# Optimization experiments

Measured on AMD Instinct MI355X. Metric: run time of the kernel, lower is better.

Reference implementation:

```python
import jax, jax.numpy as jnp
import numpy as np

EPS = 1e-5

def bn(x, g, b):
    # BatchNorm1d, training-mode batch statistics.
    axes = (0, 2) if x.ndim == 3 else (0,)
    m = jnp.mean(x, axis=axes, keepdims=True)
    v = jnp.var(x, axis=axes, keepdims=True)
    shape = (1, -1, 1) if x.ndim == 3 else (1, -1)
    return (x - m) / jnp.sqrt(v + EPS) * g.reshape(shape) + b.reshape(shape)

def conv1(x, w):
    # 1x1 conv1d == channel matmul: w [O,C], x [B,C,N]
    return jnp.einsum('oc,bcn->bon', w, x)

def knn_cov(x, local_idx, k):
    # x: [B,C,N], local_idx: [B,N] bool (local=True branch)
    B, C, N = x.shape
    xx = jnp.sum(x * x, axis=1, keepdims=True)          # [B,1,N]
    inner = -2.0 * jnp.einsum('bcn,bcm->bnm', x, x)      # [B,N,N]
    pd = -xx - inner - jnp.swapaxes(xx, 1, 2)            # neg sq dist [B,N,N]
    Min = jnp.min(pd, axis=-1)                           # [B,N]
    pd = jnp.where(local_idx[:, None, :], pd, Min[:, :, None])
    idx = jax.lax.top_k(jax.lax.stop_gradient(pd), k)[1]  # [B,N,k] nearest
    pts = jnp.swapaxes(x, 1, 2)                          # [B,N,C]
    knn_x = jax.vmap(lambda p, i: p[i])(pts, idx)        # [B,N,k,C]
    knn_x = knn_x - jnp.mean(knn_x, axis=2, keepdims=True)
    cov = jnp.einsum('bnkc,bnkd->bncd', knn_x, knn_x)    # [B,N,C,C]
    cov = cov.reshape(B, N, C * C).transpose(0, 2, 1)    # [B,C^2,N]
    return jnp.concatenate([x, cov], axis=1)             # [B,C+C^2,N]

def setup_inputs() -> dict:
    key = jax.random.key(0)
    ks = jax.random.split(key, 16)
    B, C, N, k = 4, 3, 8192, 20
    emb = 1024
    d = {}
    d['x'] = jax.random.normal(ks[0], (B, C, N), dtype=jnp.float32)
    d['local_idx'] = jax.random.randint(ks[1], (B, N), 0, 2) > 0
    d['k'] = k
    cin = C + C * C  # 12
    d['w1'] = jax.random.normal(ks[2], (64, cin), jnp.float32) * 0.1
    d['w2'] = jax.random.normal(ks[3], (64, 64), jnp.float32) * 0.1
    d['w3'] = jax.random.normal(ks[4], (64, 64), jnp.float32) * 0.1
    d['w4'] = jax.random.normal(ks[5], (128, 64), jnp.float32) * 0.1
    d['w5'] = jax.random.normal(ks[6], (emb, 128), jnp.float32) * 0.05
    for i, c in zip(range(1, 6), [64, 64, 64, 128, emb]):
        d[f'g{i}'] = jnp.ones((c,), jnp.float32)
        d[f'b{i}'] = jnp.zeros((c,), jnp.float32)
    d['lw1'] = jax.random.normal(ks[7], (512, emb), jnp.float32) * 0.03
    d['g6'] = jnp.ones((512,), jnp.float32)
    d['b6'] = jnp.zeros((512,), jnp.float32)
    d['lw2'] = jax.random.normal(ks[8], (4, 512), jnp.float32) * 0.05
    d['lb2'] = jnp.zeros((4,), jnp.float32)
    return d

def reference(x, local_idx, k, w1, w2, w3, w4, w5,
              g1, b1, g2, b2, g3, b3, g4, b4, g5, b5,
              lw1, g6, b6, lw2, lb2):
    h = knn_cov(x, local_idx, k)                 # [B,12,N]
    h = jax.nn.relu(bn(conv1(h, w1), g1, b1))
    h = jax.nn.relu(bn(conv1(h, w2), g2, b2))
    h = jax.nn.relu(bn(conv1(h, w3), g3, b3))
    h = jax.nn.relu(bn(conv1(h, w4), g4, b4))
    h = jax.nn.relu(bn(conv1(h, w5), g5, b5))    # [B,emb,N]
    h = jnp.max(h, axis=2)                        # global max pool [B,emb]
    h = jax.nn.relu(bn(h @ lw1.T, g6, b6))        # [B,512]
    # dropout: identity at eval
    return h @ lw2.T + lb2                        # [B,4]
```

## Files before the change

### kernel.cpp

```cpp
#include <hip/hip_runtime.h>

constexpr int BB = 4, NN = 8192, KNB = 20;
constexpr int BN_ = BB * NN;
constexpr float EPSV = 1e-5f;

constexpr size_t OFF_MODE  = 0;
constexpr size_t OFF_PCNT  = 16;
constexpr size_t OFF_PL    = 64;
constexpr size_t OFF_M0 = OFF_PL + 131072;
constexpr size_t OFF_S0 = OFF_M0 + 12;
constexpr size_t OFF_M1 = OFF_S0 + 144;
constexpr size_t OFF_S1 = OFF_M1 + 64;
constexpr size_t OFF_M2 = OFF_S1 + 64 * 64;
constexpr size_t OFF_S2 = OFF_M2 + 64;
constexpr size_t OFF_M3 = OFF_S2 + 64 * 64;
constexpr size_t OFF_S3 = OFF_M3 + 64;
constexpr size_t OFF_M4 = OFF_S3 + 64 * 64;
constexpr size_t OFF_S4 = OFF_M4 + 128;
constexpr size_t OFF_POOL = OFF_S4 + 128 * 128;
constexpr size_t OFF_ZEND = OFF_POOL + BB * 1024;
constexpr size_t OFF_A1 = OFF_ZEND;
constexpr size_t OFF_B1 = OFF_A1 + 64;
constexpr size_t OFF_A2 = OFF_B1 + 64;
constexpr size_t OFF_B2 = OFF_A2 + 64;
constexpr size_t OFF_A3 = OFF_B2 + 64;
constexpr size_t OFF_B3 = OFF_A3 + 64;
constexpr size_t OFF_A4 = OFF_B3 + 64;
constexpr size_t OFF_B4 = OFF_A4 + 128;
constexpr size_t OFF_A5 = OFF_B4 + 128;
constexpr size_t OFF_B5 = OFF_A5 + 1024;
constexpr size_t OFF_SH = OFF_B5 + 1024;
constexpr size_t OFF_WT1 = OFF_SH + BB * 512;
constexpr size_t OFF_WT2 = OFF_WT1 + 768;
constexpr size_t OFF_WT3 = OFF_WT2 + 4096;
constexpr size_t OFF_WT4 = OFF_WT3 + 4096;
constexpr size_t OFF_WT5_RAW = OFF_WT4 + 8192;
constexpr size_t OFF_WT5 = (OFF_WT5_RAW + 63) & ~size_t(63);
constexpr size_t OFF_H0_RAW = OFF_WT5 + 1024 * 128;
constexpr size_t OFF_H0 = (OFF_H0_RAW + 63) & ~size_t(63);
constexpr size_t OFF_H1 = OFF_H0 + (size_t)BB * 12 * NN;
constexpr size_t OFF_H2 = OFF_H1 + (size_t)BB * 64 * NN;
constexpr size_t OFF_H3 = OFF_H1;
constexpr size_t OFF_H4 = OFF_H2 + (size_t)BB * 64 * NN;
constexpr size_t OFF_P64  = OFF_H4;
constexpr size_t OFF_P128 = OFF_H1;
constexpr size_t WS_FLOATS = OFF_H4 + (size_t)BB * 128 * NN;

__device__ inline float dist3(const float4 c, float x0, float x1, float x2) {
  const float d0 = c.x - x0, d1 = c.y - x1, d2 = c.z - x2;
  return __builtin_fmaf(d0, d0, __builtin_fmaf(d1, d1, d2 * d2));
}

__global__ __launch_bounds__(256) void k_prep(const unsigned int* __restrict__ li32,
                                              int* __restrict__ mode,
                                              int* __restrict__ pcnt,
                                              float4* __restrict__ pl,
                                              const float* __restrict__ x) {
  const int b = blockIdx.x;
  const int t = threadIdx.x;
  const int lane = t & 63;
  const int w = t >> 6;
  __shared__ int s_wc[4];
  __shared__ int s_base;
  __shared__ int s_any;
  if (t == 0) { s_base = 0; s_any = 0; }
  __syncthreads();
  unsigned int any = 0;
  for (int i = t; i < 2048; i += 256) any |= (li32[b * 2048 + i] > 1u) ? 1u : 0u;
  if (any) atomicOr(&s_any, 1);
  __syncthreads();
  const int md = s_any;
  if (b == 0 && t == 0) *mode = md;
  const unsigned char* p8 = (const unsigned char*)li32;
  const float* __restrict__ xb = x + (size_t)b * 3 * NN;
  for (int j0 = 0; j0 < NN; j0 += 256) {
    const int m = j0 + t;
    const int f = md ? (p8[b * NN + m] != 0) : (li32[b * NN + m] != 0);
    const unsigned long long mask = __ballot(f);
    const int pos = __popcll(mask & ((1ull << lane) - 1ull));
    if (lane == 0) s_wc[w] = (int)__popcll(mask);
    __syncthreads();
    int off = s_base;
    for (int ww = 0; ww < w; ++ww) off += s_wc[ww];
    const int tot = s_wc[0] + s_wc[1] + s_wc[2] + s_wc[3];
    if (f) pl[(size_t)b * NN + off + pos] =
        make_float4(xb[m], xb[NN + m], xb[2 * NN + m], __int_as_float(m));
    __syncthreads();
    if (t == 0) s_base += tot;
    __syncthreads();
  }
  if (t == 0) pcnt[b] = s_base;
}

__global__ void k_wtall(const float* __restrict__ w1, const float* __restrict__ w2,
                        const float* __restrict__ w3, const float* __restrict__ w4,
                        const float* __restrict__ w5, float* __restrict__ wt1,
                        float* __restrict__ wt2, float* __restrict__ wt3,
                        float* __restrict__ wt4, float* __restrict__ wt5) {
  const int i = blockIdx.x * 256 + threadIdx.x;
  if (i < 768)        { const int o = i / 12,  c = i % 12;  wt1[c * 64 + o]  = w1[i]; }
  else if (i < 4864)  { const int j = i - 768;  const int o = j >> 6, c = j & 63;  wt2[c * 64 + o]  = w2[j]; }
  else if (i < 8960)  { const int j = i - 4864; const int o = j >> 6, c = j & 63;  wt3[c * 64 + o]  = w3[j]; }
  else if (i < 17152) { const int j = i - 8960; const int o = j >> 6, c = j & 63;  wt4[c * 128 + o] = w4[j]; }
  else if (i < 148224){ const int j = i - 17152;const int o = j >> 7, c = j & 127; wt5[c * 1024 + o] = w5[j]; }
}

__global__ __launch_bounds__(512) void k_knn(const float* __restrict__ x,
                                             const float4* __restrict__ pl,
                                             const int* __restrict__ pcnt,
                                             float* __restrict__ h0) {
  const int blk  = blockIdx.x;
  const int b    = blk >> 7;
  const int tile = blk & 127;
  const int t    = threadIdx.x;
  const int lane = t & 63;
  const int w    = __builtin_amdgcn_readfirstlane(t >> 6);
  const int n    = tile * 64 + lane;

  __shared__ float s_pool[8 * 64 * 21];
  __shared__ float s_T[64];
  __shared__ float s_red[64][13];
  __shared__ int   s_tc[64];
  __shared__ int   s_ti[64][16];
  float* __restrict__ s_dbuf  = s_pool;
  int*   __restrict__ s_dbufi = (int*)s_pool;

  const float* __restrict__ xb  = x + (size_t)b * 3 * NN;
  const float4* __restrict__ plb = pl + (size_t)b * NN;
  const int cnt = pcnt[b];
  const float xn0 = xb[n], xn1 = xb[NN + n], xn2 = xb[2 * NN + n];

  const int jlo = (cnt * w) >> 3;
  const int jhi = (cnt * (w + 1)) >> 3;

  float tk[KNB];
#pragma unroll
  for (int i = 0; i < KNB; ++i) tk[i] = 3.0e38f;

  {
    float thr = 3.0e38f;
    int bc = 0;
    for (int j = jlo; j < jhi; ++j) {
      const float4 c = plb[j];
      const float d = dist3(c, xn0, xn1, xn2);
      if (d < thr) { s_dbuf[bc * 512 + t] = d; ++bc; }
      if (__any(bc == 8)) {
        for (int i = 0; i < bc; ++i) {
          float dv = s_dbuf[i * 512 + t];
          if (dv < tk[KNB - 1]) {
#pragma unroll
            for (int q2 = 0; q2 < KNB; ++q2) {
              const float lo = fminf(tk[q2], dv);
              dv = fmaxf(tk[q2], dv);
              tk[q2] = lo;
            }
          }
        }
        bc = 0;
        thr = tk[KNB - 1];
      }
    }
    for (int i = 0; i < bc; ++i) {
      float dv = s_dbuf[i * 512 + t];
      if (dv < tk[KNB - 1]) {
#pragma unroll
        for (int q2 = 0; q2 < KNB; ++q2) {
          const float lo = fminf(tk[q2], dv);
          dv = fmaxf(tk[q2], dv);
          tk[q2] = lo;
        }
      }
    }
  }
  __syncthreads();

  {
    const int base = (w * 64 + lane) * 21;
#pragma unroll
    for (int i = 0; i < KNB; ++i) s_pool[base + i] = tk[i];
    s_pool[base + KNB] = 3.0e38f;
  }
  __syncthreads();

  if (w == 0) {
    int i0 = 0, i1 = 0, i2 = 0, i3 = 0, i4 = 0, i5 = 0, i6 = 0, i7 = 0;
    float T = 0.f;
    for (int c = 0; c < KNB; ++c) {
      const float v0 = s_pool[(0 * 64 + lane) * 21 + i0];
      const float v1 = s_pool[(1 * 64 + lane) * 21 + i1];
      const float v2 = s_pool[(2 * 64 + lane) * 21 + i2];
      const float v3 = s_pool[(3 * 64 + lane) * 21 + i3];
      const float v4 = s_pool[(4 * 64 + lane) * 21 + i4];
      const float v5 = s_pool[(5 * 64 + lane) * 21 + i5];
      const float v6 = s_pool[(6 * 64 + lane) * 21 + i6];
      const float v7 = s_pool[(7 * 64 + lane) * 21 + i7];
      float best = fminf(fminf(fminf(v0, v1), fminf(v2, v3)),
                         fminf(fminf(v4, v5), fminf(v6, v7)));
      int adv, taken;
      adv = (v0 == best) ? 1 : 0;           i0 += adv; taken = adv;
      adv = (!taken && v1 == best) ? 1 : 0; i1 += adv; taken |= adv;
      adv = (!taken && v2 == best) ? 1 : 0; i2 += adv; taken |= adv;
      adv = (!taken && v3 == best) ? 1 : 0; i3 += adv; taken |= adv;
      adv = (!taken && v4 == best) ? 1 : 0; i4 += adv; taken |= adv;
      adv = (!taken && v5 == best) ? 1 : 0; i5 += adv; taken |= adv;
      adv = (!taken && v6 == best) ? 1 : 0; i6 += adv; taken |= adv;
      adv = (!taken && v7 == best) ? 1 : 0; i7 += adv;
      T = best;
    }
    s_T[lane] = T;
    s_tc[lane] = 0;
  }
  __syncthreads();
  const float T = s_T[lane];

  float sx = 0, sy = 0, sz = 0;
  float xx = 0, xy = 0, xz = 0, yy = 0, yz = 0, zz = 0;
  float clf = 0;
  {
    s_dbufi[t] = jlo;
    int bc = 0;
    for (int j = jlo; j < jhi; ++j) {
      const float4 c = plb[j];
      const float d = dist3(c, xn0, xn1, xn2);
      if (d <= T) { s_dbufi[bc * 512 + t] = j; ++bc; }
      if (__any(bc == 8)) {
        int jj[8]; float4 cc[8];
#pragma unroll
        for (int i = 0; i < 8; ++i) {
          const int slot = (i < bc) ? i : 0;
          jj[i] = s_dbufi[slot * 512 + t];
          cc[i] = plb[jj[i]];
        }
#pragma unroll
        for (int i = 0; i < 8; ++i) {
          if (i < bc) {
            const float d2 = dist3(cc[i], xn0, xn1, xn2);
            if (d2 < T) {
              clf += 1.f;
              sx += cc[i].x; sy += cc[i].y; sz += cc[i].z;
              xx = __builtin_fmaf(cc[i].x, cc[i].x, xx);
              xy = __builtin_fmaf(cc[i].x, cc[i].y, xy);
              xz = __builtin_fmaf(cc[i].x, cc[i].z, xz);
              yy = __builtin_fmaf(cc[i].y, cc[i].y, yy);
              yz = __builtin_fmaf(cc[i].y, cc[i].z, yz);
              zz = __builtin_fmaf(cc[i].z, cc[i].z, zz);
            } else {
              const int pos = atomicAdd(&s_tc[lane], 1);
              if (pos < 16) s_ti[lane][pos] = jj[i];
            }
          }
        }
        bc = 0;
      }
    }
    if (bc > 0) {
      int jj[8]; float4 cc[8];
#pragma unroll
      for (int i = 0; i < 8; ++i) {
        const int slot = (i < bc) ? i : 0;
        jj[i] = s_dbufi[slot * 512 + t];
        cc[i] = plb[jj[i]];
      }
#pragma unroll
      for (int i = 0; i < 8; ++i) {
        if (i < bc) {
          const float d2 = dist3(cc[i], xn0, xn1, xn2);
          if (d2 < T) {
            clf += 1.f;
            sx += cc[i].x; sy += cc[i].y; sz += cc[i].z;
            xx = __builtin_fmaf(cc[i].x, cc[i].x, xx);
            xy = __builtin_fmaf(cc[i].x, cc[i].y, xy);
            xz = __builtin_fmaf(cc[i].x, cc[i].z, xz);
            yy = __builtin_fmaf(cc[i].y, cc[i].y, yy);
            yz = __builtin_fmaf(cc[i].y, cc[i].z, yz);
            zz = __builtin_fmaf(cc[i].z, cc[i].z, zz);
          } else {
            const int pos = atomicAdd(&s_tc[lane], 1);
            if (pos < 16) s_ti[lane][pos] = jj[i];
          }
        }
      }
    }
  }
  __syncthreads();
  {
    const int base = (w * 64 + lane) * 13;
    s_pool[base + 0] = sx; s_pool[base + 1] = sy; s_pool[base + 2] = sz;
    s_pool[base + 3] = xx; s_pool[base + 4] = xy; s_pool[base + 5] = xz;
    s_pool[base + 6] = yy; s_pool[base + 7] = yz; s_pool[base + 8] = zz;
    s_pool[base + 9] = clf;
  }
  __syncthreads();
  {
    const int q = t & 63, a = t >> 6;
    float s = 0.f;
#pragma unroll
    for (int wv = 0; wv < 8; ++wv) s += s_pool[(wv * 64 + q) * 13 + a];
    s_red[q][a] = s;
    if (a < 2) {
      const int a2 = a + 8;
      float s2 = 0.f;
#pragma unroll
      for (int wv = 0; wv < 8; ++wv) s2 += s_pool[(wv * 64 + q) * 13 + a2];
      s_red[q][a2] = s2;
    }
  }
  __syncthreads();

  if (w == 0) {
    float fsx = s_red[lane][0], fsy = s_red[lane][1], fsz = s_red[lane][2];
    float fxx = s_red[lane][3], fxy = s_red[lane][4], fxz = s_red[lane][5];
    float fyy = s_red[lane][6], fyz = s_red[lane][7], fzz = s_red[lane][8];
    const int cl = (int)s_red[lane][9];
    const int r = KNB - cl;
    const int tc = min(s_tc[lane], 16);
    int kk = cl;
    int prev = -1;
    for (int s = 0; s < r; ++s) {
      int best = 0x7fffffff;
      for (int u = 0; u < tc; ++u) {
        const int mi2 = s_ti[lane][u];
        if (mi2 > prev && mi2 < best) best = mi2;
      }
      if (best == 0x7fffffff) break;
      const float4 pp = plb[best];
      fsx += pp.x; fsy += pp.y; fsz += pp.z;
      fxx = __builtin_fmaf(pp.x, pp.x, fxx);
      fxy = __builtin_fmaf(pp.x, pp.y, fxy);
      fxz = __builtin_fmaf(pp.x, pp.z, fxz);
      fyy = __builtin_fmaf(pp.y, pp.y, fyy);
      fyz = __builtin_fmaf(pp.y, pp.z, fyz);
      fzz = __builtin_fmaf(pp.z, pp.z, fzz);
      prev = best;
      ++kk;
    }
    const float kf = (float)max(kk, 1);
    const float inv = 1.0f / kf;
    const float mx = fsx * inv, my = fsy * inv, mz = fsz * inv;
    const float c00 = fxx - kf * mx * mx;
    const float c01 = fxy - kf * mx * my;
    const float c02 = fxz - kf * mx * mz;
    const float c11 = fyy - kf * my * my;
    const float c12 = fyz - kf * my * mz;
    const float c22 = fzz - kf * mz * mz;
    float* __restrict__ op = h0 + (size_t)b * 12 * NN + n;
    op[0] = xn0; op[(size_t)NN] = xn1; op[(size_t)2 * NN] = xn2;
    op[(size_t)3 * NN] = c00; op[(size_t)4 * NN]  = c01; op[(size_t)5 * NN]  = c02;
    op[(size_t)6 * NN] = c01; op[(size_t)7 * NN]  = c11; op[(size_t)8 * NN]  = c12;
    op[(size_t)9 * NN] = c02; op[(size_t)10 * NN] = c12; op[(size_t)11 * NN] = c22;
  }
}

template <int C>
__global__ __launch_bounds__(256) void k_stats_small(const float* __restrict__ h,
                                                     float* __restrict__ mo,
                                                     float* __restrict__ So) {
  constexpr int NP  = C * (C + 1) / 2;
  constexpr int KPT = (NP + 255) / 256;
  __shared__ float tile[C][65];
  const int t = threadIdx.x;
  float acc[KPT];
#pragma unroll
  for (int e = 0; e < KPT; ++e) acc[e] = 0.f;
  float accm = 0.f;
  for (int tl = blockIdx.x; tl < BN_ / 64; tl += gridDim.x) {
    const int b  = tl >> 7;
    const int p0 = (tl & 127) * 64;
    for (int idx = t; idx < C * 64; idx += 256) {
      const int c = idx >> 6, p = idx & 63;
      tile[c][p] = h[((size_t)b * C + c) * NN + p0 + p];
    }
    __syncthreads();
    {
      int ii = 0, rem = t;
#pragma unroll
      for (int e = 0; e < KPT; ++e) {
        const int lin = t + 256 * e;
        if (lin < NP) {
          while (rem >= C - ii) { rem -= C - ii; ++ii; }
          const int jj = ii + rem;
          float s = 0.f;
#pragma unroll 8
          for (int p = 0; p < 64; ++p) s = __builtin_fmaf(tile[ii][p], tile[jj][p], s);
          acc[e] += s;
        }
        rem += 256;
      }
    }
    if (t < C) {
      float s = 0.f;
#pragma unroll 8
      for (int p = 0; p < 64; ++p) s += tile[t][p];
      accm += s;
    }
    __syncthreads();
  }
  {
    int ii = 0, rem = t;
#pragma unroll
    for (int e = 0; e < KPT; ++e) {
      const int lin = t + 256 * e;
      if (lin < NP) {
        while (rem >= C - ii) { rem -= C - ii; ++ii; }
        atomicAdd(&So[ii * C + ii + rem], acc[e]);
      }
      rem += 256;
    }
  }
  if (t < C) atomicAdd(&mo[t], accm);
}

template <int C>
__global__ __launch_bounds__(512) void k_stats(const float* __restrict__ h,
                                               float* __restrict__ part) {
  constexpr int G      = (C == 128) ? 8 : 4;
  constexpr int NPB    = 136 * G * G;
  constexpr int ROWLEN = NPB + C;
  constexpr int STR    = C + 4;
  __shared__ float ht[128][STR];
  __shared__ float red[136][G * G];
  const int t   = threadIdx.x;
  const int blk = blockIdx.x;
  const int b   = blk >> 6;
  const int p0  = (blk & 63) * 128;
  for (int i = t; i < C * 128; i += 512) {
    const int c = i >> 7, p = i & 127;
    ht[p][c] = h[((size_t)b * C + c) * NN + p0 + p];
  }
  __syncthreads();
  const int s  = t >> 8;
  const int pb = t & 255;
  const int bi = pb & 15;
  const int bj = pb >> 4;
  const bool act = (bi <= bj);
  float acc[G * G];
#pragma unroll
  for (int g = 0; g < G * G; ++g) acc[g] = 0.f;
  if (act) {
    for (int p = s * 64; p < s * 64 + 64; ++p) {
      float a[G], bv[G];
      *(float4*)&a[0] = *(const float4*)&ht[p][bi * G];
      *(float4*)&bv[0] = *(const float4*)&ht[p][bj * G];
      if constexpr (G == 8) {
        *(float4*)&a[4] = *(const float4*)&ht[p][bi * G + 4];
        *(float4*)&bv[4] = *(const float4*)&ht[p][bj * G + 4];
      }
#pragma unroll
      for (int gi = 0; gi < G; ++gi)
#pragma unroll
        for (int gj = 0; gj < G; ++gj)
          acc[gi * G + gj] = __builtin_fmaf(a[gi], bv[gj], acc[gi * G + gj]);
    }
  }
  const int rank = bj * (bj + 1) / 2 + bi;
  if (s == 1 && act) {
#pragma unroll
    for (int g = 0; g < G * G; ++g) red[rank][g] = acc[g];
  }
  __syncthreads();
  float* __restrict__ prow = part + (size_t)blk * ROWLEN;
  if (s == 0 && act) {
#pragma unroll
    for (int g = 0; g < G * G; g += 4) {
      float4 v;
      v.x = acc[g + 0] + red[rank][g + 0];
      v.y = acc[g + 1] + red[rank][g + 1];
      v.z = acc[g + 2] + red[rank][g + 2];
      v.w = acc[g + 3] + red[rank][g + 3];
      *(float4*)&prow[rank * G * G + g] = v;
    }
  }
  if (t < C) {
    float sm = 0.f;
#pragma unroll 8
    for (int p = 0; p < 128; ++p) sm += ht[p][t];
    prow[NPB + t] = sm;
  }
}

template <int C>
__global__ __launch_bounds__(256) void k_sred(const float* __restrict__ part,
                                              float* __restrict__ mo,
                                              float* __restrict__ So) {
  constexpr int G      = (C == 128) ? 8 : 4;
  constexpr int GG     = G * G;
  constexpr int NPB    = 136 * GG;
  constexpr int ROWLEN = NPB + C;
  const int e = blockIdx.x * 256 + threadIdx.x;
  if (e >= ROWLEN) return;
  const float* __restrict__ p = part + e;
  float s = 0.f;
#pragma unroll 8
  for (int r = 0; r < 256; ++r) s += p[(size_t)r * ROWLEN];
  if (e < NPB) {
    const int rank = e / GG;
    const int g    = e - rank * GG;
    int bj = 0;
    while ((bj + 1) * (bj + 2) / 2 <= rank) ++bj;
    const int bi = rank - bj * (bj + 1) / 2;
    const int gi = g / G, gj = g - gi * G;
    So[(bi * G + gi) * C + (bj * G + gj)] = s;
  } else {
    mo[e - NPB] = s;
  }
}

template <int CIN, int COUT>
__global__ __launch_bounds__(256) void k_solve(const float* __restrict__ w, const float* __restrict__ g,
                        const float* __restrict__ bb, const float* __restrict__ m,
                        const float* __restrict__ S, float* __restrict__ A,
                        float* __restrict__ Bc) {
  const int wv   = threadIdx.x >> 6;
  const int lane = threadIdx.x & 63;
  const int o    = blockIdx.x * 4 + wv;
  if (o >= COUT) return;
  const float* __restrict__ wr = w + (size_t)o * CIN;
  float mu = 0.f;
  for (int i = lane; i < CIN; i += 64) mu = __builtin_fmaf(wr[i], m[i], mu);
  float e2 = 0.f;
#pragma unroll 4
  for (int lin = lane; lin < CIN * CIN; lin += 64) {
    const int i = lin / CIN;
    const int j = lin - i * CIN;
    const int lo = min(i, j), hi = max(i, j);
    e2 = __builtin_fmaf(wr[i] * wr[j], S[lo * CIN + hi], e2);
  }
#pragma unroll
  for (int off = 32; off >= 1; off >>= 1) {
    mu += __shfl_xor(mu, off, 64);
    e2 += __shfl_xor(e2, off, 64);
  }
  if (lane == 0) {
    mu *= (1.0f / BN_);
    e2 *= (1.0f / BN_);
    const float var = e2 - mu * mu;
    const float a = g[o] / sqrtf(var + EPSV);
    A[o] = a;
    Bc[o] = bb[o] - mu * a;
  }
}

template <int CIN, int COUT>
__global__ __launch_bounds__(256) void k_cgemm(const float* __restrict__ hin,
                                               const float* __restrict__ wt,
                                               const float* __restrict__ A,
                                               const float* __restrict__ Bc,
                                               float* __restrict__ outp) {
  constexpr int nOT = COUT / 64;
  __shared__ float tin[CIN][64];
  __shared__ float twt[CIN][64];
  const int blk = blockIdx.x;
  const int ot  = blk % nOT;
  const int pt  = blk / nOT;
  const int b   = pt >> 7;
  const int p0  = (pt & 127) * 64;
  const int o0  = ot * 64;
  const int t   = threadIdx.x;

  for (int i = t; i < CIN * 16; i += 256) {
    const int c = i >> 4, sgm = i & 15;
    *(float4*)&tin[c][sgm * 4] =
        *(const float4*)&hin[((size_t)b * CIN + c) * NN + p0 + sgm * 4];
    *(float4*)&twt[c][sgm * 4] =
        *(const float4*)&wt[(size_t)c * COUT + o0 + sgm * 4];
  }
  __syncthreads();

  const int to = t & 15;
  const int tp = t >> 4;
  float acc[4][4];
#pragma unroll
  for (int i = 0; i < 4; ++i)
#pragma unroll
    for (int j = 0; j < 4; ++j) acc[i][j] = 0.f;

#pragma unroll 4
  for (int c = 0; c < CIN; ++c) {
    const float4 av = *(const float4*)&twt[c][to * 4];
    const float4 pv = *(const float4*)&tin[c][tp * 4];
    const float aa[4] = {av.x, av.y, av.z, av.w};
    const float pp[4] = {pv.x, pv.y, pv.z, pv.w};
#pragma unroll
    for (int i = 0; i < 4; ++i)
#pragma unroll
      for (int j = 0; j < 4; ++j)
        acc[i][j] = __builtin_fmaf(aa[i], pp[j], acc[i][j]);
  }

#pragma unroll
  for (int i = 0; i < 4; ++i) {
    const int o = o0 + to * 4 + i;
    const float Ao = A[o], Bo = Bc[o];
    float4 vv;
    vv.x = fmaxf(__builtin_fmaf(acc[i][0], Ao, Bo), 0.f);
    vv.y = fmaxf(__builtin_fmaf(acc[i][1], Ao, Bo), 0.f);
    vv.z = fmaxf(__builtin_fmaf(acc[i][2], Ao, Bo), 0.f);
    vv.w = fmaxf(__builtin_fmaf(acc[i][3], Ao, Bo), 0.f);
    *(float4*)&outp[((size_t)b * COUT + o) * NN + p0 + tp * 4] = vv;
  }
}

__global__ __launch_bounds__(256) void k_cgemm5(const float* __restrict__ h4,
                                                const float* __restrict__ wt,
                                                const float* __restrict__ A,
                                                const float* __restrict__ Bc,
                                                float* __restrict__ pooled) {
  __shared__ float tin[64][64];
  __shared__ float twt[64][128];
  const int blk = blockIdx.x;
  const int ot  = blk & 7;
  const int pt  = blk >> 3;
  const int b   = pt >> 7;
  const int p0  = (pt & 127) * 64;
  const int o0  = ot * 128;
  const int t   = threadIdx.x;
  const int to  = t & 15;
  const int tp  = t >> 4;

  float acc[8][4];
#pragma unroll
  for (int i = 0; i < 8; ++i)
#pragma unroll
    for (int j = 0; j < 4; ++j) acc[i][j] = 0.f;

  for (int kc = 0; kc < 128; kc += 64) {
    if (kc) __syncthreads();
    for (int i = t; i < 64 * 16; i += 256) {
      const int c = i >> 4, sg = i & 15;
      *(float4*)&tin[c][sg * 4] =
          *(const float4*)&h4[((size_t)b * 128 + kc + c) * NN + p0 + sg * 4];
    }
    for (int i = t; i < 64 * 32; i += 256) {
      const int c = i >> 5, sg = i & 31;
      *(float4*)&twt[c][sg * 4] =
          *(const float4*)&wt[(size_t)(kc + c) * 1024 + o0 + sg * 4];
    }
    __syncthreads();
#pragma unroll 2
    for (int c = 0; c < 64; ++c) {
      float w8[8], p4[4];
      *(float4*)&w8[0] = *(const float4*)&twt[c][to * 8];
      *(float4*)&w8[4] = *(const float4*)&twt[c][to * 8 + 4];
      *(float4*)&p4[0] = *(const float4*)&tin[c][tp * 4];
#pragma unroll
      for (int i = 0; i < 8; ++i)
#pragma unroll
        for (int j = 0; j < 4; ++j)
          acc[i][j] = __builtin_fmaf(w8[i], p4[j], acc[i][j]);
    }
  }

  float mx[8];
#pragma unroll
  for (int i = 0; i < 8; ++i) {
    const int o = o0 + to * 8 + i;
    const float a = A[o], bo = Bc[o];
    float v0 = fmaxf(__builtin_fmaf(acc[i][0], a, bo), 0.f);
    float v1 = fmaxf(__builtin_fmaf(acc[i][1], a, bo), 0.f);
    float v2 = fmaxf(__builtin_fmaf(acc[i][2], a, bo), 0.f);
    float v3 = fmaxf(__builtin_fmaf(acc[i][3], a, bo), 0.f);
    float m = fmaxf(fmaxf(v0, v1), fmaxf(v2, v3));
    m = fmaxf(m, __shfl_xor(m, 16, 64));
    m = fmaxf(m, __shfl_xor(m, 32, 64));
    mx[i] = m;
  }
  float* s_part = &twt[0][0];
  __syncthreads();
  const int lane = t & 63, w = t >> 6;
  if (lane < 16) {
#pragma unroll
    for (int i = 0; i < 8; ++i) s_part[w * 128 + to * 8 + i] = mx[i];
  }
  __syncthreads();
  if (t < 128) {
    const float mm = fmaxf(fmaxf(s_part[t], s_part[128 + t]),
                           fmaxf(s_part[256 + t], s_part[384 + t]));
    atomicMax((int*)pooled + (size_t)b * 1024 + o0 + t, __float_as_int(mm));
  }
}

__global__ __launch_bounds__(256) void k_head1(const float* __restrict__ pooled, const float* __restrict__ lw1,
                        const float* __restrict__ g6, const float* __restrict__ b6,
                        float* __restrict__ sh) {
  const int wv   = threadIdx.x >> 6;
  const int lane = threadIdx.x & 63;
  const int o    = blockIdx.x * 4 + wv;
  const float* __restrict__ wr = lw1 + (size_t)o * 1024;
  float y0 = 0, y1 = 0, y2 = 0, y3 = 0;
  for (int c = lane; c < 1024; c += 64) {
    const float wvv = wr[c];
    y0 = __builtin_fmaf(wvv, pooled[c], y0);
    y1 = __builtin_fmaf(wvv, pooled[1024 + c], y1);
    y2 = __builtin_fmaf(wvv, pooled[2048 + c], y2);
    y3 = __builtin_fmaf(wvv, pooled[3072 + c], y3);
  }
#pragma unroll
  for (int off = 32; off >= 1; off >>= 1) {
    y0 += __shfl_xor(y0, off, 64);
    y1 += __shfl_xor(y1, off, 64);
    y2 += __shfl_xor(y2, off, 64);
    y3 += __shfl_xor(y3, off, 64);
  }
  if (lane == 0) {
    const float mu = 0.25f * (y0 + y1 + y2 + y3);
    const float d0 = y0 - mu, d1 = y1 - mu, d2 = y2 - mu, d3 = y3 - mu;
    const float var = 0.25f * (d0 * d0 + d1 * d1 + d2 * d2 + d3 * d3);
    const float a = g6[o] / sqrtf(var + EPSV);
    const float bc = b6[o];
    sh[o]        = fmaxf(__builtin_fmaf(d0, a, bc), 0.f);
    sh[512 + o]  = fmaxf(__builtin_fmaf(d1, a, bc), 0.f);
    sh[1024 + o] = fmaxf(__builtin_fmaf(d2, a, bc), 0.f);
    sh[1536 + o] = fmaxf(__builtin_fmaf(d3, a, bc), 0.f);
  }
}

__global__ void k_head2(const float* __restrict__ sh, const float* __restrict__ lw2,
                        const float* __restrict__ lb2, float* __restrict__ out) {
  const int wv   = threadIdx.x >> 6;
  const int lane = threadIdx.x & 63;
  float s0 = 0, s1 = 0, s2 = 0, s3 = 0;
  for (int c = lane; c < 512; c += 64) {
    const float h = sh[wv * 512 + c];
    s0 = __builtin_fmaf(lw2[c], h, s0);
    s1 = __builtin_fmaf(lw2[512 + c], h, s1);
    s2 = __builtin_fmaf(lw2[1024 + c], h, s2);
    s3 = __builtin_fmaf(lw2[1536 + c], h, s3);
  }
#pragma unroll
  for (int off = 32; off >= 1; off >>= 1) {
    s0 += __shfl_xor(s0, off, 64);
    s1 += __shfl_xor(s1, off, 64);
    s2 += __shfl_xor(s2, off, 64);
    s3 += __shfl_xor(s3, off, 64);
  }
  if (lane == 0) {
    out[wv * 4 + 0] = s0 + lb2[0];
    out[wv * 4 + 1] = s1 + lb2[1];
    out[wv * 4 + 2] = s2 + lb2[2];
    out[wv * 4 + 3] = s3 + lb2[3];
  }
}

extern "C" void kernel_launch(void* const* d_in, const int* in_sizes, int n_in,
                              void* d_out, int out_size, void* d_ws, size_t ws_size,
                              hipStream_t stream) {
  (void)in_sizes; (void)n_in; (void)out_size; (void)ws_size;
  const float* x    = (const float*)d_in[0];
  const void*  lidx = d_in[1];
  const float* w1 = (const float*)d_in[3];
  const float* w2 = (const float*)d_in[4];
  const float* w3 = (const float*)d_in[5];
  const float* w4 = (const float*)d_in[6];
  const float* w5 = (const float*)d_in[7];
  const float* g1 = (const float*)d_in[8],  *b1 = (const float*)d_in[9];
  const float* g2 = (const float*)d_in[10], *b2 = (const float*)d_in[11];
  const float* g3 = (const float*)d_in[12], *b3 = (const float*)d_in[13];
  const float* g4 = (const float*)d_in[14], *b4 = (const float*)d_in[15];
  const float* g5 = (const float*)d_in[16], *b5 = (const float*)d_in[17];
  const float* lw1 = (const float*)d_in[18];
  const float* g6 = (const float*)d_in[19], *b6 = (const float*)d_in[20];
  const float* lw2 = (const float*)d_in[21], *lb2 = (const float*)d_in[22];
  float* out = (float*)d_out;
  float* ws  = (float*)d_ws;

  hipMemsetAsync(ws + OFF_M0, 0, (OFF_ZEND - OFF_M0) * sizeof(float), stream);

  k_prep<<<4, 256, 0, stream>>>((const unsigned int*)lidx, (int*)(ws + OFF_MODE),
                                (int*)(ws + OFF_PCNT), (float4*)(ws + OFF_PL), x);
  k_wtall<<<579, 256, 0, stream>>>(w1, w2, w3, w4, w5, ws + OFF_WT1, ws + OFF_WT2,
                                   ws + OFF_WT3, ws + OFF_WT4, ws + OFF_WT5);
  k_knn<<<512, 512, 0, stream>>>(x, (const float4*)(ws + OFF_PL),
                                 (const int*)(ws + OFF_PCNT), ws + OFF_H0);

  k_stats_small<12><<<128, 256, 0, stream>>>(ws + OFF_H0, ws + OFF_M0, ws + OFF_S0);
  k_solve<12, 64><<<16, 256, 0, stream>>>(w1, g1, b1, ws + OFF_M0, ws + OFF_S0,
                                          ws + OFF_A1, ws + OFF_B1);
  k_cgemm<12, 64><<<512, 256, 0, stream>>>(ws + OFF_H0, ws + OFF_WT1,
                                           ws + OFF_A1, ws + OFF_B1, ws + OFF_H1);

  k_stats<64><<<256, 512, 0, stream>>>(ws + OFF_H1, ws + OFF_P64);
  k_sred<64><<<9, 256, 0, stream>>>(ws + OFF_P64, ws + OFF_M1, ws + OFF_S1);
  k_solve<64, 64><<<16, 256, 0, stream>>>(w2, g2, b2, ws + OFF_M1, ws + OFF_S1,
                                          ws + OFF_A2, ws + OFF_B2);
  k_cgemm<64, 64><<<512, 256, 0, stream>>>(ws + OFF_H1, ws + OFF_WT2,
                                           ws + OFF_A2, ws + OFF_B2, ws + OFF_H2);

  k_stats<64><<<256, 512, 0, stream>>>(ws + OFF_H2, ws + OFF_P64);
  k_sred<64><<<9, 256, 0, stream>>>(ws + OFF_P64, ws + OFF_M2, ws + OFF_S2);
  k_solve<64, 64><<<16, 256, 0, stream>>>(w3, g3, b3, ws + OFF_M2, ws + OFF_S2,
                                          ws + OFF_A3, ws + OFF_B3);
  k_cgemm<64, 64><<<512, 256, 0, stream>>>(ws + OFF_H2, ws + OFF_WT3,
                                           ws + OFF_A3, ws + OFF_B3, ws + OFF_H3);

  k_stats<64><<<256, 512, 0, stream>>>(ws + OFF_H3, ws + OFF_P64);
  k_sred<64><<<9, 256, 0, stream>>>(ws + OFF_P64, ws + OFF_M3, ws + OFF_S3);
  k_solve<64, 128><<<32, 256, 0, stream>>>(w4, g4, b4, ws + OFF_M3, ws + OFF_S3,
                                           ws + OFF_A4, ws + OFF_B4);
  k_cgemm<64, 128><<<1024, 256, 0, stream>>>(ws + OFF_H3, ws + OFF_WT4,
                                             ws + OFF_A4, ws + OFF_B4, ws + OFF_H4);

  k_stats<128><<<256, 512, 0, stream>>>(ws + OFF_H4, ws + OFF_P128);
  k_sred<128><<<35, 256, 0, stream>>>(ws + OFF_P128, ws + OFF_M4, ws + OFF_S4);
  k_solve<128, 1024><<<256, 256, 0, stream>>>(w5, g5, b5, ws + OFF_M4, ws + OFF_S4,
                                              ws + OFF_A5, ws + OFF_B5);
  k_cgemm5<<<4096, 256, 0, stream>>>(ws + OFF_H4, ws + OFF_WT5,
                                     ws + OFF_A5, ws + OFF_B5, ws + OFF_POOL);

  k_head1<<<128, 256, 0, stream>>>(ws + OFF_POOL, lw1, g6, b6, ws + OFF_SH);
  k_head2<<<1, 256, 0, stream>>>(ws + OFF_SH, lw2, lb2, out);
}
```

Before: 586.6 us.

## Split kNN candidate scan 16 ways with 16 queries per block

Restructures the kNN kernel so each 256-thread block handles 16 query points, with 16 threads per query each scanning a sixteenth of the local candidate list, launched as 2048 blocks instead of 512. The per-part top-k lists are merged with a 16-way merge, and the partial covariance sums are reduced over 16 parts. The aim is more blocks and better load balance across CUs and lower per-thread serial scan length. The cost is a larger serial merge done by only 16 active lanes, and mixed query/part mapping within a wavefront, which changes load coalescing and divergence.

New measurement: 661.9 us. 1.13x slower.

```diff
diff --git a/kernel.cpp b/kernel.cpp
--- a/kernel.cpp
+++ b/kernel.cpp
@@ -105,23 +105,23 @@
   else if (i < 148224){ const int j = i - 17152;const int o = j >> 7, c = j & 127; wt5[c * 1024 + o] = w5[j]; }
 }
 
-__global__ __launch_bounds__(512) void k_knn(const float* __restrict__ x,
+__global__ __launch_bounds__(256) void k_knn(const float* __restrict__ x,
                                              const float4* __restrict__ pl,
                                              const int* __restrict__ pcnt,
                                              float* __restrict__ h0) {
   const int blk  = blockIdx.x;
-  const int b    = blk >> 7;
-  const int tile = blk & 127;
+  const int b    = blk >> 9;
+  const int tile = blk & 511;
   const int t    = threadIdx.x;
-  const int lane = t & 63;
-  const int w    = __builtin_amdgcn_readfirstlane(t >> 6);
-  const int n    = tile * 64 + lane;
-
-  __shared__ float s_pool[8 * 64 * 21];
-  __shared__ float s_T[64];
-  __shared__ float s_red[64][13];
-  __shared__ int   s_tc[64];
-  __shared__ int   s_ti[64][16];
+  const int qid  = t & 15;
+  const int part = t >> 4;
+  const int n    = tile * 16 + qid;
+
+  __shared__ float s_pool[256 * 21];
+  __shared__ float s_T[16];
+  __shared__ float s_red[16][13];
+  __shared__ int   s_tc[16];
+  __shared__ int   s_ti[16][24];
   float* __restrict__ s_dbuf  = s_pool;
   int*   __restrict__ s_dbufi = (int*)s_pool;
 
@@ -130,8 +130,8 @@
   const int cnt = pcnt[b];
   const float xn0 = xb[n], xn1 = xb[NN + n], xn2 = xb[2 * NN + n];
 
-  const int jlo = (cnt * w) >> 3;
-  const int jhi = (cnt * (w + 1)) >> 3;
+  const int jlo = (cnt * part) >> 4;
+  const int jhi = (cnt * (part + 1)) >> 4;
 
   float tk[KNB];
 #pragma unroll
@@ -140,13 +140,14 @@
   {
     float thr = 3.0e38f;
     int bc = 0;
+#pragma unroll 2
     for (int j = jlo; j < jhi; ++j) {
       const float4 c = plb[j];
       const float d = dist3(c, xn0, xn1, xn2);
-      if (d < thr) { s_dbuf[bc * 512 + t] = d; ++bc; }
+      if (d < thr) { s_dbuf[bc * 256 + t] = d; ++bc; }
       if (__any(bc == 8)) {
         for (int i = 0; i < bc; ++i) {
-          float dv = s_dbuf[i * 512 + t];
+          float dv = s_dbuf[i * 256 + t];
           if (dv < tk[KNB - 1]) {
 #pragma unroll
             for (int q2 = 0; q2 < KNB; ++q2) {
@@ -161,7 +162,7 @@
       }
     }
     for (int i = 0; i < bc; ++i) {
-      float dv = s_dbuf[i * 512 + t];
+      float dv = s_dbuf[i * 256 + t];
       if (dv < tk[KNB - 1]) {
 #pragma unroll
         for (int q2 = 0; q2 < KNB; ++q2) {
@@ -175,43 +176,62 @@
   __syncthreads();
 
   {
-    const int base = (w * 64 + lane) * 21;
+    const int base = t * 21;
 #pragma unroll
     for (int i = 0; i < KNB; ++i) s_pool[base + i] = tk[i];
     s_pool[base + KNB] = 3.0e38f;
   }
   __syncthreads();
 
-  if (w == 0) {
-    int i0 = 0, i1 = 0, i2 = 0, i3 = 0, i4 = 0, i5 = 0, i6 = 0, i7 = 0;
+  if (t < 16) {
+    int i0=0,i1=0,i2=0,i3=0,i4=0,i5=0,i6=0,i7=0;
+    int i8=0,i9=0,i10=0,i11=0,i12=0,i13=0,i14=0,i15=0;
     float T = 0.f;
     for (int c = 0; c < KNB; ++c) {
-      const float v0 = s_pool[(0 * 64 + lane) * 21 + i0];
-      const float v1 = s_pool[(1 * 64 + lane) * 21 + i1];
-      const float v2 = s_pool[(2 * 64 + lane) * 21 + i2];
-      const float v3 = s_pool[(3 * 64 + lane) * 21 + i3];
-      const float v4 = s_pool[(4 * 64 + lane) * 21 + i4];
-      const float v5 = s_pool[(5 * 64 + lane) * 21 + i5];
-      const float v6 = s_pool[(6 * 64 + lane) * 21 + i6];
-      const float v7 = s_pool[(7 * 64 + lane) * 21 + i7];
-      float best = fminf(fminf(fminf(v0, v1), fminf(v2, v3)),
-                         fminf(fminf(v4, v5), fminf(v6, v7)));
+      const float v0  = s_pool[( 0*16 + t)*21 + i0];
+      const float v1  = s_pool[( 1*16 + t)*21 + i1];
+      const float v2  = s_pool[( 2*16 + t)*21 + i2];
+      const float v3  = s_pool[( 3*16 + t)*21 + i3];
+      const float v4  = s_pool[( 4*16 + t)*21 + i4];
+      const float v5  = s_pool[( 5*16 + t)*21 + i5];
+      const float v6  = s_pool[( 6*16 + t)*21 + i6];
+      const float v7  = s_pool[( 7*16 + t)*21 + i7];
+      const float v8  = s_pool[( 8*16 + t)*21 + i8];
+      const float v9  = s_pool[( 9*16 + t)*21 + i9];
+      const float v10 = s_pool[(10*16 + t)*21 + i10];
+      const float v11 = s_pool[(11*16 + t)*21 + i11];
+      const float v12 = s_pool[(12*16 + t)*21 + i12];
+      const float v13 = s_pool[(13*16 + t)*21 + i13];
+      const float v14 = s_pool[(14*16 + t)*21 + i14];
+      const float v15 = s_pool[(15*16 + t)*21 + i15];
+      float best = fminf(fminf(fminf(fminf(v0,v1),fminf(v2,v3)),
+                               fminf(fminf(v4,v5),fminf(v6,v7))),
+                         fminf(fminf(fminf(v8,v9),fminf(v10,v11)),
+                               fminf(fminf(v12,v13),fminf(v14,v15))));
       int adv, taken;
-      adv = (v0 == best) ? 1 : 0;           i0 += adv; taken = adv;
-      adv = (!taken && v1 == best) ? 1 : 0; i1 += adv; taken |= adv;
-      adv = (!taken && v2 == best) ? 1 : 0; i2 += adv; taken |= adv;
-      adv = (!taken && v3 == best) ? 1 : 0; i3 += adv; taken |= adv;
-      adv = (!taken && v4 == best) ? 1 : 0; i4 += adv; taken |= adv;
-      adv = (!taken && v5 == best) ? 1 : 0; i5 += adv; taken |= adv;
-      adv = (!taken && v6 == best) ? 1 : 0; i6 += adv; taken |= adv;
-      adv = (!taken && v7 == best) ? 1 : 0; i7 += adv;
+      adv = (v0  == best) ? 1 : 0;           i0  += adv; taken  = adv;
+      adv = (!taken && v1  == best) ? 1 : 0; i1  += adv; taken |= adv;
+      adv = (!taken && v2  == best) ? 1 : 0; i2  += adv; taken |= adv;
+      adv = (!taken && v3  == best) ? 1 : 0; i3  += adv; taken |= adv;
+      adv = (!taken && v4  == best) ? 1 : 0; i4  += adv; taken |= adv;
+      adv = (!taken && v5  == best) ? 1 : 0; i5  += adv; taken |= adv;
+      adv = (!taken && v6  == best) ? 1 : 0; i6  += adv; taken |= adv;
+      adv = (!taken && v7  == best) ? 1 : 0; i7  += adv; taken |= adv;
+      adv = (!taken && v8  == best) ? 1 : 0; i8  += adv; taken |= adv;
+      adv = (!taken && v9  == best) ? 1 : 0; i9  += adv; taken |= adv;
+      adv = (!taken && v10 == best) ? 1 : 0; i10 += adv; taken |= adv;
+      adv = (!taken && v11 == best) ? 1 : 0; i11 += adv; taken |= adv;
+      adv = (!taken && v12 == best) ? 1 : 0; i12 += adv; taken |= adv;
+      adv = (!taken && v13 == best) ? 1 : 0; i13 += adv; taken |= adv;
+      adv = (!taken && v14 == best) ? 1 : 0; i14 += adv; taken |= adv;
+      adv = (!taken && v15 == best) ? 1 : 0; i15 += adv;
       T = best;
     }
-    s_T[lane] = T;
-    s_tc[lane] = 0;
-  }
-  __syncthreads();
-  const float T = s_T[lane];
+    s_T[t] = T;
+    s_tc[t] = 0;
+  }
+  __syncthreads();
+  const float T = s_T[qid];
 
   float sx = 0, sy = 0, sz = 0;
   float xx = 0, xy = 0, xz = 0, yy = 0, yz = 0, zz = 0;
@@ -222,13 +242,13 @@
     for (int j = jlo; j < jhi; ++j) {
       const float4 c = plb[j];
       const float d = dist3(c, xn0, xn1, xn2);
-      if (d <= T) { s_dbufi[bc * 512 + t] = j; ++bc; }
+      if (d <= T) { s_dbufi[bc * 256 + t] = j; ++bc; }
       if (__any(bc == 8)) {
         int jj[8]; float4 cc[8];
 #pragma unroll
         for (int i = 0; i < 8; ++i) {
           const int slot = (i < bc) ? i : 0;
-          jj[i] = s_dbufi[slot * 512 + t];
+          jj[i] = s_dbufi[slot * 256 + t];
           cc[i] = plb[jj[i]];
         }
 #pragma unroll
@@ -245,8 +265,8 @@
               yz = __builtin_fmaf(cc[i].y, cc[i].z, yz);
               zz = __builtin_fmaf(cc[i].z, cc[i].z, zz);
             } else {
-              const int pos = atomicAdd(&s_tc[lane], 1);
-              if (pos < 16) s_ti[lane][pos] = jj[i];
+              const int pos = atomicAdd(&s_tc[qid], 1);
+              if (pos < 24) s_ti[qid][pos] = jj[i];
             }
           }
         }
@@ -258,7 +278,7 @@
 #pragma unroll
       for (int i = 0; i < 8; ++i) {
         const int slot = (i < bc) ? i : 0;
-        jj[i] = s_dbufi[slot * 512 + t];
+        jj[i] = s_dbufi[slot * 256 + t];
         cc[i] = plb[jj[i]];
       }
 #pragma unroll
@@ -275,8 +295,8 @@
             yz = __builtin_fmaf(cc[i].y, cc[i].z, yz);
             zz = __builtin_fmaf(cc[i].z, cc[i].z, zz);
           } else {
-            const int pos = atomicAdd(&s_tc[lane], 1);
-            if (pos < 16) s_ti[lane][pos] = jj[i];
+            const int pos = atomicAdd(&s_tc[qid], 1);
+            if (pos < 24) s_ti[qid][pos] = jj[i];
           }
         }
       }
@@ -284,7 +304,7 @@
   }
   __syncthreads();
   {
-    const int base = (w * 64 + lane) * 13;
+    const int base = t * 13;
     s_pool[base + 0] = sx; s_pool[base + 1] = sy; s_pool[base + 2] = sz;
     s_pool[base + 3] = xx; s_pool[base + 4] = xy; s_pool[base + 5] = xz;
     s_pool[base + 6] = yy; s_pool[base + 7] = yz; s_pool[base + 8] = zz;
@@ -292,34 +312,29 @@
   }
   __syncthreads();
   {
-    const int q = t & 63, a = t >> 6;
-    float s = 0.f;
-#pragma unroll
-    for (int wv = 0; wv < 8; ++wv) s += s_pool[(wv * 64 + q) * 13 + a];
-    s_red[q][a] = s;
-    if (a < 2) {
-      const int a2 = a + 8;
-      float s2 = 0.f;
-#pragma unroll
-      for (int wv = 0; wv < 8; ++wv) s2 += s_pool[(wv * 64 + q) * 13 + a2];
-      s_red[q][a2] = s2;
-    }
-  }
-  __syncthreads();
-
-  if (w == 0) {
-    float fsx = s_red[lane][0], fsy = s_red[lane][1], fsz = s_red[lane][2];
-    float fxx = s_red[lane][3], fxy = s_red[lane][4], fxz = s_red[lane][5];
-    float fyy = s_red[lane][6], fyz = s_red[lane][7], fzz = s_red[lane][8];
-    const int cl = (int)s_red[lane][9];
+    const int q2 = t & 15, a = t >> 4;
+    if (a < 13) {
+      float s = 0.f;
+#pragma unroll
+      for (int p = 0; p < 16; ++p) s += s_pool[(p * 16 + q2) * 13 + a];
+      s_red[q2][a] = s;
+    }
+  }
+  __syncthreads();
+
+  if (t < 16) {
+    float fsx = s_red[t][0], fsy = s_red[t][1], fsz = s_red[t][2];
+    float fxx = s_red[t][3], fxy = s_red[t][4], fxz = s_red[t][5];
+    float fyy = s_red[t][6], fyz = s_red[t][7], fzz = s_red[t][8];
+    const int cl = (int)s_red[t][9];
     const int r = KNB - cl;
-    const int tc = min(s_tc[lane], 16);
+    const int tc = min(s_tc[t], 24);
     int kk = cl;
     int prev = -1;
     for (int s = 0; s < r; ++s) {
       int best = 0x7fffffff;
       for (int u = 0; u < tc; ++u) {
-        const int mi2 = s_ti[lane][u];
+        const int mi2 = s_ti[t][u];
         if (mi2 > prev && mi2 < best) best = mi2;
       }
       if (best == 0x7fffffff) break;
@@ -343,8 +358,9 @@
     const float c11 = fyy - kf * my * my;
     const float c12 = fyz - kf * my * mz;
     const float c22 = fzz - kf * mz * mz;
+    const float qx0 = xb[n], qx1 = xb[NN + n], qx2 = xb[2 * NN + n];
     float* __restrict__ op = h0 + (size_t)b * 12 * NN + n;
-    op[0] = xn0; op[(size_t)NN] = xn1; op[(size_t)2 * NN] = xn2;
+    op[0] = qx0; op[(size_t)NN] = qx1; op[(size_t)2 * NN] = qx2;
     op[(size_t)3 * NN] = c00; op[(size_t)4 * NN]  = c01; op[(size_t)5 * NN]  = c02;
     op[(size_t)6 * NN] = c01; op[(size_t)7 * NN]  = c11; op[(size_t)8 * NN]  = c12;
     op[(size_t)9 * NN] = c02; op[(size_t)10 * NN] = c12; op[(size_t)11 * NN] = c22;
@@ -769,8 +785,8 @@
                                 (int*)(ws + OFF_PCNT), (float4*)(ws + OFF_PL), x);
   k_wtall<<<579, 256, 0, stream>>>(w1, w2, w3, w4, w5, ws + OFF_WT1, ws + OFF_WT2,
                                    ws + OFF_WT3, ws + OFF_WT4, ws + OFF_WT5);
-  k_knn<<<512, 512, 0, stream>>>(x, (const float4*)(ws + OFF_PL),
-                                 (const int*)(ws + OFF_PCNT), ws + OFF_H0);
+  k_knn<<<2048, 256, 0, stream>>>(x, (const float4*)(ws + OFF_PL),
+                                  (const int*)(ws + OFF_PCNT), ws + OFF_H0);
 
   k_stats_small<12><<<128, 256, 0, stream>>>(ws + OFF_H0, ws + OFF_M0, ws + OFF_S0);
   k_solve<12, 64><<<16, 256, 0, stream>>>(w1, g1, b1, ws + OFF_M0, ws + OFF_S0,
```

## Unroll kNN distance scans, drop index buffering, enlarge conv5 point tile

Applied to the files above, without the earlier changes.

The kNN first pass now unrolls the candidate scan by four, loading and testing four points per iteration. The second pass stops buffering candidate indices and re-gathering their coordinates: it accumulates points below the threshold directly and records only exact ties, with tie capacity raised from 16 to 24. The final conv5+maxpool GEMM doubles its point tile to 128, so each thread computes an 8x8 register block and half as many blocks are launched. Weight reuse per block goes up, at the cost of more registers and LDS per block, which may lower occupancy.

Result: faster. 550.2 us (median of 2 runs) (-6.2%).

```diff
diff --git a/kernel.cpp b/kernel.cpp
--- a/kernel.cpp
+++ b/kernel.cpp
@@ -121,9 +121,8 @@
   __shared__ float s_T[64];
   __shared__ float s_red[64][13];
   __shared__ int   s_tc[64];
-  __shared__ int   s_ti[64][16];
-  float* __restrict__ s_dbuf  = s_pool;
-  int*   __restrict__ s_dbufi = (int*)s_pool;
+  __shared__ int   s_ti[64][24];
+  float* __restrict__ s_dbuf = s_pool;
 
   const float* __restrict__ xb  = x + (size_t)b * 3 * NN;
   const float4* __restrict__ plb = pl + (size_t)b * NN;
@@ -140,11 +139,19 @@
   {
     float thr = 3.0e38f;
     int bc = 0;
-    for (int j = jlo; j < jhi; ++j) {
-      const float4 c = plb[j];
-      const float d = dist3(c, xn0, xn1, xn2);
-      if (d < thr) { s_dbuf[bc * 512 + t] = d; ++bc; }
-      if (__any(bc == 8)) {
+    int j = jlo;
+    for (; j + 3 < jhi; j += 4) {
+      const float4 c0 = plb[j],     c1 = plb[j + 1];
+      const float4 c2 = plb[j + 2], c3 = plb[j + 3];
+      const float d0 = dist3(c0, xn0, xn1, xn2);
+      const float d1 = dist3(c1, xn0, xn1, xn2);
+      const float d2 = dist3(c2, xn0, xn1, xn2);
+      const float d3 = dist3(c3, xn0, xn1, xn2);
+      if (d0 < thr) { s_dbuf[bc * 512 + t] = d0; ++bc; }
+      if (d1 < thr) { s_dbuf[bc * 512 + t] = d1; ++bc; }
+      if (d2 < thr) { s_dbuf[bc * 512 + t] = d2; ++bc; }
+      if (d3 < thr) { s_dbuf[bc * 512 + t] = d3; ++bc; }
+      if (__any(bc >= 8)) {
         for (int i = 0; i < bc; ++i) {
           float dv = s_dbuf[i * 512 + t];
           if (dv < tk[KNB - 1]) {
@@ -159,6 +166,11 @@
         bc = 0;
         thr = tk[KNB - 1];
       }
+    }
+    for (; j < jhi; ++j) {
+      const float4 c = plb[j];
+      const float d = dist3(c, xn0, xn1, xn2);
+      if (d < thr) { s_dbuf[bc * 512 + t] = d; ++bc; }
     }
     for (int i = 0; i < bc; ++i) {
       float dv = s_dbuf[i * 512 + t];
@@ -217,68 +229,62 @@
   float xx = 0, xy = 0, xz = 0, yy = 0, yz = 0, zz = 0;
   float clf = 0;
   {
-    s_dbufi[t] = jlo;
-    int bc = 0;
-    for (int j = jlo; j < jhi; ++j) {
+    int j = jlo;
+    for (; j + 3 < jhi; j += 4) {
+      const float4 c0 = plb[j],     c1 = plb[j + 1];
+      const float4 c2 = plb[j + 2], c3 = plb[j + 3];
+      const float d0 = dist3(c0, xn0, xn1, xn2);
+      const float d1 = dist3(c1, xn0, xn1, xn2);
+      const float d2 = dist3(c2, xn0, xn1, xn2);
+      const float d3 = dist3(c3, xn0, xn1, xn2);
+      if (d0 < T) {
+        clf += 1.f; sx += c0.x; sy += c0.y; sz += c0.z;
+        xx = __builtin_fmaf(c0.x, c0.x, xx); xy = __builtin_fmaf(c0.x, c0.y, xy);
+        xz = __builtin_fmaf(c0.x, c0.z, xz); yy = __builtin_fmaf(c0.y, c0.y, yy);
+        yz = __builtin_fmaf(c0.y, c0.z, yz); zz = __builtin_fmaf(c0.z, c0.z, zz);
+      } else if (d0 == T) {
+        const int pos = atomicAdd(&s_tc[lane], 1);
+        if (pos < 24) s_ti[lane][pos] = j;
+      }
+      if (d1 < T) {
+        clf += 1.f; sx += c1.x; sy += c1.y; sz += c1.z;
+        xx = __builtin_fmaf(c1.x, c1.x, xx); xy = __builtin_fmaf(c1.x, c1.y, xy);
+        xz = __builtin_fmaf(c1.x, c1.z, xz); yy = __builtin_fmaf(c1.y, c1.y, yy);
+        yz = __builtin_fmaf(c1.y, c1.z, yz); zz = __builtin_fmaf(c1.z, c1.z, zz);
+      } else if (d1 == T) {
+        const int pos = atomicAdd(&s_tc[lane], 1);
+        if (pos < 24) s_ti[lane][pos] = j + 1;
+      }
+      if (d2 < T) {
+        clf += 1.f; sx += c2.x; sy += c2.y; sz += c2.z;
+        xx = __builtin_fmaf(c2.x, c2.x, xx); xy = __builtin_fmaf(c2.x, c2.y, xy);
+        xz = __builtin_fmaf(c2.x, c2.z, xz); yy = __builtin_fmaf(c2.y, c2.y, yy);
+        yz = __builtin_fmaf(c2.y, c2.z, yz); zz = __builtin_fmaf(c2.z, c2.z, zz);
+      } else if (d2 == T) {
+        const int pos = atomicAdd(&s_tc[lane], 1);
+        if (pos < 24) s_ti[lane][pos] = j + 2;
+      }
+      if (d3 < T) {
+        clf += 1.f; sx += c3.x; sy += c3.y; sz += c3.z;
+        xx = __builtin_fmaf(c3.x, c3.x, xx); xy = __builtin_fmaf(c3.x, c3.y, xy);
+        xz = __builtin_fmaf(c3.x, c3.z, xz); yy = __builtin_fmaf(c3.y, c3.y, yy);
+        yz = __builtin_fmaf(c3.y, c3.z, yz); zz = __builtin_fmaf(c3.z, c3.z, zz);
+      } else if (d3 == T) {
+        const int pos = atomicAdd(&s_tc[lane], 1);
+        if (pos < 24) s_ti[lane][pos] = j + 3;
+      }
+    }
+    for (; j < jhi; ++j) {
       const float4 c = plb[j];
       const float d = dist3(c, xn0, xn1, xn2);
-      if (d <= T) { s_dbufi[bc * 512 + t] = j; ++bc; }
-      if (__any(bc == 8)) {
-        int jj[8]; float4 cc[8];
-#pragma unroll
-        for (int i = 0; i < 8; ++i) {
-          const int slot = (i < bc) ? i : 0;
-          jj[i] = s_dbufi[slot * 512 + t];
-          cc[i] = plb[jj[i]];
-        }
-#pragma unroll
-        for (int i = 0; i < 8; ++i) {
-          if (i < bc) {
-            const float d2 = dist3(cc[i], xn0, xn1, xn2);
-            if (d2 < T) {
-              clf += 1.f;
-              sx += cc[i].x; sy += cc[i].y; sz += cc[i].z;
-              xx = __builtin_fmaf(cc[i].x, cc[i].x, xx);
-              xy = __builtin_fmaf(cc[i].x, cc[i].y, xy);
-              xz = __builtin_fmaf(cc[i].x, cc[i].z, xz);
-              yy = __builtin_fmaf(cc[i].y, cc[i].y, yy);
-              yz = __builtin_fmaf(cc[i].y, cc[i].z, yz);
-              zz = __builtin_fmaf(cc[i].z, cc[i].z, zz);
-            } else {
-              const int pos = atomicAdd(&s_tc[lane], 1);
-              if (pos < 16) s_ti[lane][pos] = jj[i];
-            }
-          }
-        }
-        bc = 0;
-      }
-    }
-    if (bc > 0) {
-      int jj[8]; float4 cc[8];
-#pragma unroll
-      for (int i = 0; i < 8; ++i) {
-        const int slot = (i < bc) ? i : 0;
-        jj[i] = s_dbufi[slot * 512 + t];
-        cc[i] = plb[jj[i]];
-      }
-#pragma unroll
-      for (int i = 0; i < 8; ++i) {
-        if (i < bc) {
-          const float d2 = dist3(cc[i], xn0, xn1, xn2);
-          if (d2 < T) {
-            clf += 1.f;
-            sx += cc[i].x; sy += cc[i].y; sz += cc[i].z;
-            xx = __builtin_fmaf(cc[i].x, cc[i].x, xx);
-            xy = __builtin_fmaf(cc[i].x, cc[i].y, xy);
-            xz = __builtin_fmaf(cc[i].x, cc[i].z, xz);
-            yy = __builtin_fmaf(cc[i].y, cc[i].y, yy);
-            yz = __builtin_fmaf(cc[i].y, cc[i].z, yz);
-            zz = __builtin_fmaf(cc[i].z, cc[i].z, zz);
-          } else {
-            const int pos = atomicAdd(&s_tc[lane], 1);
-            if (pos < 16) s_ti[lane][pos] = jj[i];
-          }
-        }
+      if (d < T) {
+        clf += 1.f; sx += c.x; sy += c.y; sz += c.z;
+        xx = __builtin_fmaf(c.x, c.x, xx); xy = __builtin_fmaf(c.x, c.y, xy);
+        xz = __builtin_fmaf(c.x, c.z, xz); yy = __builtin_fmaf(c.y, c.y, yy);
+        yz = __builtin_fmaf(c.y, c.z, yz); zz = __builtin_fmaf(c.z, c.z, zz);
+      } else if (d == T) {
+        const int pos = atomicAdd(&s_tc[lane], 1);
+        if (pos < 24) s_ti[lane][pos] = j;
       }
     }
   }
@@ -313,7 +319,7 @@
     float fyy = s_red[lane][6], fyz = s_red[lane][7], fzz = s_red[lane][8];
     const int cl = (int)s_red[lane][9];
     const int r = KNB - cl;
-    const int tc = min(s_tc[lane], 16);
+    const int tc = min(s_tc[lane], 24);
     int kk = cl;
     int prev = -1;
     for (int s = 0; s < r; ++s) {
@@ -605,48 +611,46 @@
                                                 const float* __restrict__ A,
                                                 const float* __restrict__ Bc,
                                                 float* __restrict__ pooled) {
-  __shared__ float tin[64][64];
+  __shared__ float tin[64][128];
   __shared__ float twt[64][128];
   const int blk = blockIdx.x;
   const int ot  = blk & 7;
   const int pt  = blk >> 3;
-  const int b   = pt >> 7;
-  const int p0  = (pt & 127) * 64;
+  const int b   = pt >> 6;
+  const int p0  = (pt & 63) * 128;
   const int o0  = ot * 128;
   const int t   = threadIdx.x;
   const int to  = t & 15;
   const int tp  = t >> 4;
 
-  float acc[8][4];
+  float acc[8][8];
 #pragma unroll
   for (int i = 0; i < 8; ++i)
 #pragma unroll
-    for (int j = 0; j < 4; ++j) acc[i][j] = 0.f;
+    for (int j = 0; j < 8; ++j) acc[i][j] = 0.f;
 
   for (int kc = 0; kc < 128; kc += 64) {
     if (kc) __syncthreads();
-    for (int i = t; i < 64 * 16; i += 256) {
-      const int c = i >> 4, sg = i & 15;
+    for (int i = t; i < 64 * 32; i += 256) {
+      const int c = i >> 5, sg = i & 31;
       *(float4*)&tin[c][sg * 4] =
           *(const float4*)&h4[((size_t)b * 128 + kc + c) * NN + p0 + sg * 4];
-    }
-    for (int i = t; i < 64 * 32; i += 256) {
-      const int c = i >> 5, sg = i & 31;
       *(float4*)&twt[c][sg * 4] =
           *(const float4*)&wt[(size_t)(kc + c) * 1024 + o0 + sg * 4];
     }
     __syncthreads();
 #pragma unroll 2
     for (int c = 0; c < 64; ++c) {
-      float w8[8], p4[4];
+      float w8[8], p8[8];
       *(float4*)&w8[0] = *(const float4*)&twt[c][to * 8];
       *(float4*)&w8[4] = *(const float4*)&twt[c][to * 8 + 4];
-      *(float4*)&p4[0] = *(const float4*)&tin[c][tp * 4];
+      *(float4*)&p8[0] = *(const float4*)&tin[c][tp * 8];
+      *(float4*)&p8[4] = *(const float4*)&tin[c][tp * 8 + 4];
 #pragma unroll
       for (int i = 0; i < 8; ++i)
 #pragma unroll
-        for (int j = 0; j < 4; ++j)
-          acc[i][j] = __builtin_fmaf(w8[i], p4[j], acc[i][j]);
+        for (int j = 0; j < 8; ++j)
+          acc[i][j] = __builtin_fmaf(w8[i], p8[j], acc[i][j]);
     }
   }
 
@@ -655,11 +659,11 @@
   for (int i = 0; i < 8; ++i) {
     const int o = o0 + to * 8 + i;
     const float a = A[o], bo = Bc[o];
-    float v0 = fmaxf(__builtin_fmaf(acc[i][0], a, bo), 0.f);
-    float v1 = fmaxf(__builtin_fmaf(acc[i][1], a, bo), 0.f);
-    float v2 = fmaxf(__builtin_fmaf(acc[i][2], a, bo), 0.f);
-    float v3 = fmaxf(__builtin_fmaf(acc[i][3], a, bo), 0.f);
-    float m = fmaxf(fmaxf(v0, v1), fmaxf(v2, v3));
+    float m = 0.f;
+#pragma unroll
+    for (int j = 0; j < 8; ++j)
+      m = fmaxf(m, __builtin_fmaf(acc[i][j], a, bo));
+    m = fmaxf(m, 0.f);
     m = fmaxf(m, __shfl_xor(m, 16, 64));
     m = fmaxf(m, __shfl_xor(m, 32, 64));
     mx[i] = m;
@@ -803,7 +807,7 @@
   k_sred<128><<<35, 256, 0, stream>>>(ws + OFF_P128, ws + OFF_M4, ws + OFF_S4);
   k_solve<128, 1024><<<256, 256, 0, stream>>>(w5, g5, b5, ws + OFF_M4, ws + OFF_S4,
                                               ws + OFF_A5, ws + OFF_B5);
-  k_cgemm5<<<4096, 256, 0, stream>>>(ws + OFF_H4, ws + OFF_WT5,
+  k_cgemm5<<<2048, 256, 0, stream>>>(ws + OFF_H4, ws + OFF_WT5,
                                      ws + OFF_A5, ws + OFF_B5, ws + OFF_POOL);
 
   k_head1<<<128, 256, 0, stream>>>(ws + OFF_POOL, lw1, g6, b6, ws + OFF_SH);
```
